# Kernel optimization log

Measured on AMD Instinct MI355X. Metric: run time of the kernel, lower is better.

## Reference

```python
import jax, jax.numpy as jnp
import numpy as np

NUM_HEADS = 8


def setup_inputs() -> dict:
    key = jax.random.key(0)
    k0, k1, k2 = jax.random.split(key, 3)
    B, C, D, H, W = 2, 256, 16, 16, 8
    x = jax.random.normal(k0, (B, C, D, H, W), dtype=jnp.float32)
    # 1x1x1 Conv3d weights are pointwise linear maps over channels
    w_qkv = jax.random.normal(k1, (3 * C, C), dtype=jnp.float32) * 0.02
    b_qkv = jnp.zeros((3 * C,), dtype=jnp.float32)
    w_out = jax.random.normal(k2, (C, C), dtype=jnp.float32) * 0.02
    b_out = jnp.zeros((C,), dtype=jnp.float32)
    return {"x": x, "w_qkv": w_qkv, "b_qkv": b_qkv, "w_out": w_out, "b_out": b_out}


def reference(x, w_qkv, b_qkv, w_out, b_out):
    b, c, d, h, w = x.shape
    nh = NUM_HEADS
    hd = c // nh
    scale = hd ** (-0.5)
    n = d * h * w
    xf = x.reshape(b, c, n)  # flatten spatial volume to N tokens
    # to_qkv: pointwise conv == channel-mixing matmul
    qkv = jnp.einsum('oc,bcn->bon', w_qkv, xf) + b_qkv[None, :, None]
    # torch: view(b, H, 3*hd, N) then chunk(3, dim=2) -> per-head channel grouping
    qkv = qkv.reshape(b, nh, 3 * hd, n)
    q, k, v = jnp.split(qkv, 3, axis=2)  # each (b, nh, hd, n)
    sim = jnp.einsum('bhcn,bhcm->bhnm', q, k) * scale  # (b, nh, N, N)
    attn = jax.nn.softmax(sim, axis=-1)
    out = jnp.einsum('bhnm,bhcm->bhcn', attn, v)  # (b, nh, hd, N)
    out = out.reshape(b, c, n)
    out = jnp.einsum('oc,bcn->bon', w_out, out) + b_out[None, :, None]
    return x + out.reshape(b, c, d, h, w)
```

## Files before the change

kernel.cpp:

```cpp
#include <hip/hip_runtime.h>
#include <hip/hip_bf16.h>
#include <math.h>

#define BB 2
#define CC 256
#define NH 8
#define HD 32
#define NN 2048
#define KSPAN 1024
#define QBLK 64
#define KTILE 64
#define NITER (KSPAN / KTILE)
#define QK_SCALE 0.25500917f

typedef __attribute__((ext_vector_type(8))) short short8;
typedef __attribute__((ext_vector_type(8))) unsigned short ushort8;
typedef __attribute__((ext_vector_type(4))) float f32x4;

__device__ inline unsigned short f2bf(float f) {
    __hip_bfloat16 h = __float2bfloat16(f);
    return __builtin_bit_cast(unsigned short, h);
}
__device__ inline int kperm(int k) {
    return 32 * (k >> 5) + 16 * ((k >> 2) & 1) + 4 * ((k >> 3) & 3) + (k & 3);
}
__device__ inline int xcd_chunk(int orig, int nwg) {
    int q = nwg >> 3, r = nwg & 7, x = orig & 7, s = orig >> 3;
    return (x < r ? x * (q + 1) : r * (q + 1) + (x - r) * q) + s;
}

__global__ __launch_bounds__(256) void qkv_mfma(const float* __restrict__ x,
                                                const float* __restrict__ wq,
                                                const float* __restrict__ bias,
                                                unsigned short* __restrict__ qt,
                                                unsigned short* __restrict__ ktt,
                                                unsigned short* __restrict__ vt) {
    const int l = xcd_chunk(blockIdx.x, 768);
    const int m0 = (l % 12) * 64;
    const int xtile = l / 12;
    const int n0 = (xtile & 31) * 64;
    const int b = xtile >> 5;
    const int t = threadIdx.x, lane = t & 63, wid = t >> 6;
    const int g = lane >> 4, ln = lane & 15;
    __shared__ __align__(16) unsigned short Aw[4][64][36];
    __shared__ __align__(16) unsigned short Bx[4][64][36];
    f32x4 acc[4] = {};

    const int sm = t & 63, sch = t >> 6;
    const int pc = t >> 4, pn = t & 15;
    const int c0 = pc * 8, nl = pn * 4;
    const float* xb = x + (size_t)b * CC * NN + n0;

    for (int kh = 0; kh < 2; ++kh) {
        __syncthreads();
        {
            const float* wsrc = wq + (size_t)(m0 + sm) * CC + kh * 128 + sch * 32;
            float wv[32];
#pragma unroll
            for (int j = 0; j < 8; ++j) *(float4*)&wv[j * 4] = *(const float4*)&wsrc[j * 4];
#pragma unroll
            for (int j2 = 0; j2 < 4; ++j2) {
                ushort8 p;
#pragma unroll
                for (int e = 0; e < 8; ++e) p[e] = f2bf(wv[j2 * 8 + e]);
                *(ushort8*)&Aw[sch][sm][j2 * 8] = p;
            }
        }
        {
            const float* xsrc = xb + (size_t)(kh * 128 + c0) * NN + nl;
            float xv[8][4];
#pragma unroll
            for (int i = 0; i < 8; ++i) *(float4*)&xv[i][0] = *(const float4*)&xsrc[(size_t)i * NN];
#pragma unroll
            for (int i2 = 0; i2 < 4; ++i2) {
                ushort8 p;
#pragma unroll
                for (int e = 0; e < 8; ++e) p[e] = f2bf(xv[e][i2]);
                *(ushort8*)&Bx[pc >> 2][nl + i2][(pc & 3) * 8] = p;
            }
        }
        __syncthreads();
#pragma unroll
        for (int ks = 0; ks < 4; ++ks) {
            short8 aW = *(const short8*)&Aw[ks][wid * 16 + ln][g * 8];
#pragma unroll
            for (int nt = 0; nt < 4; ++nt) {
                short8 bX = *(const short8*)&Bx[ks][nt * 16 + ln][g * 8];
                acc[nt] = __builtin_amdgcn_mfma_f32_16x16x32_bf16(aW, bX, acc[nt], 0, 0, 0);
            }
        }
    }
    __syncthreads();
    unsigned short (*Tqk)[64][40] = (unsigned short (*)[64][40])&Aw[0][0][0];
    unsigned short (*Tv)[32][72]  = (unsigned short (*)[32][72])&Bx[0][0][0];
    {
        const int grp = wid >> 1;
        const int cl0 = (wid & 1) * 16 + 4 * g;
        const int gm0 = m0 + grp * 32;
        const int gtype = (gm0 % 96) >> 5;
        const float sc = (gtype == 0) ? QK_SCALE : 1.0f;
        float bv[4];
#pragma unroll
        for (int r = 0; r < 4; ++r) bv[r] = bias[gm0 + cl0 + r];
        if (gtype == 2) {
#pragma unroll
            for (int nt = 0; nt < 4; ++nt)
#pragma unroll
                for (int r = 0; r < 4; ++r)
                    Tv[grp][cl0 + r][nt * 16 + ln] = f2bf(acc[nt][r] + bv[r]);
        } else {
#pragma unroll
            for (int nt = 0; nt < 4; ++nt)
#pragma unroll
                for (int r = 0; r < 4; ++r)
                    Tqk[grp][nt * 16 + ln][cl0 + r] = f2bf((acc[nt][r] + bv[r]) * sc);
        }
    }
    __syncthreads();
#pragma unroll
    for (int grp2 = 0; grp2 < 2; ++grp2) {
        const int gm = m0 + grp2 * 32;
        const int gtype = (gm % 96) >> 5;
        const int head = gm / 96;
        if (gtype == 2) {
            const int cl = t >> 3, n8 = (t & 7) * 8;
            ushort8 v = *(const ushort8*)&Tv[grp2][cl][n8];
            *(ushort8*)&vt[((size_t)(b * NH + head) * HD + cl) * NN + n0 + n8] = v;
        } else {
            unsigned short* dst = (gtype == 0) ? qt : ktt;
            const int nr = t >> 2, c8 = (t & 3) * 8;
            ushort8 v = *(const ushort8*)&Tqk[grp2][nr][c8];
            *(ushort8*)&dst[((size_t)(b * NH + head) * NN + n0 + nr) * HD + c8] = v;
        }
    }
}

__global__ __launch_bounds__(512) void attn_mfma(const unsigned short* __restrict__ Qt,
                                                 const unsigned short* __restrict__ Kt,
                                                 const unsigned short* __restrict__ Vt,
                                                 unsigned short* __restrict__ aout_t) {
    const int l = xcd_chunk(blockIdx.x, 512);
    const int n0 = (l & 31) * QBLK;
    const int bh = l >> 5;
    const int h = bh & 7, b = bh >> 3;
    const int t = threadIdx.x;
    const int lane = t & 63, wid = t >> 6;
    const int g = lane >> 4, ln = lane & 15;
    const int qg = wid & 3, whalf = wid >> 2;

    __shared__ __align__(16) unsigned short Qs[QBLK][40];
    __shared__ __align__(16) unsigned short Ks[2][2][KTILE][40];
    __shared__ __align__(16) unsigned short Vs[2][2][HD][72];

    const unsigned short* qb = Qt + ((size_t)(b * NH + h) * NN + n0) * HD;
    const unsigned short* kb = Kt + (size_t)(b * NH + h) * NN * HD;
    const unsigned short* vb = Vt + (size_t)(b * NH + h) * HD * NN;

    if (t < 256) {
        int q = t >> 2, ch = (t & 3) * 8;
        *(ushort8*)&Qs[q][ch] = *(const ushort8*)&qb[(size_t)q * HD + ch];
    }
    __syncthreads();
    const short8 bQ = *(const short8*)&Qs[qg * 16 + ln][g * 8];

    const int th = t & 255, sthalf = t >> 8;
    const int sk = th >> 2, sch = (th & 3) * 8;
    const int rowK = kperm(sk);
    const int vcc = th >> 3, vn = (th & 7) * 8;
    const size_t hbase = (size_t)sthalf * KSPAN;

    ushort8 kpreA = *(const ushort8*)&kb[(hbase + 0 * KTILE + sk) * HD + sch];
    ushort8 vpreA = *(const ushort8*)&vb[(size_t)vcc * NN + hbase + 0 * KTILE + vn];
    ushort8 kpreB = *(const ushort8*)&kb[(hbase + 1 * KTILE + sk) * HD + sch];
    ushort8 vpreB = *(const ushort8*)&vb[(size_t)vcc * NN + hbase + 1 * KTILE + vn];

    float l_run = 0.f;
    f32x4 oacc[2];
    const f32x4 zero4 = {0.f, 0.f, 0.f, 0.f};
    oacc[0] = zero4; oacc[1] = zero4;

    auto compute_tile = [&](int buf) {
        f32x4 sacc[4];
        __builtin_amdgcn_s_setprio(1);
#pragma unroll
        for (int t8 = 0; t8 < 4; ++t8) {
            short8 aK = *(const short8*)&Ks[whalf][buf][t8 * 16 + ln][g * 8];
            sacc[t8] = __builtin_amdgcn_mfma_f32_16x16x32_bf16(aK, bQ, zero4, 0, 0, 0);
        }
        __builtin_amdgcn_s_setprio(0);

#pragma unroll
        for (int t8 = 0; t8 < 4; ++t8) {
            sacc[t8][0] = exp2f(sacc[t8][0]);
            sacc[t8][1] = exp2f(sacc[t8][1]);
            sacc[t8][2] = exp2f(sacc[t8][2]);
            sacc[t8][3] = exp2f(sacc[t8][3]);
        }
        float ps[4];
#pragma unroll
        for (int t8 = 0; t8 < 4; ++t8)
            ps[t8] = (sacc[t8][0] + sacc[t8][1]) + (sacc[t8][2] + sacc[t8][3]);
        l_run += (ps[0] + ps[1]) + (ps[2] + ps[3]);

        short8 aP[2];
#pragma unroll
        for (int kc = 0; kc < 2; ++kc)
#pragma unroll
            for (int u = 0; u < 2; ++u)
#pragma unroll
                for (int r = 0; r < 4; ++r)
                    aP[kc][u * 4 + r] = (short)f2bf(sacc[2 * kc + u][r]);

        __builtin_amdgcn_s_setprio(1);
#pragma unroll
        for (int kc = 0; kc < 2; ++kc) {
            short8 bV0 = *(const short8*)&Vs[whalf][buf][ln][kc * 32 + g * 8];
            short8 bV1 = *(const short8*)&Vs[whalf][buf][16 + ln][kc * 32 + g * 8];
            oacc[0] = __builtin_amdgcn_mfma_f32_16x16x32_bf16(aP[kc], bV0, oacc[0], 0, 0, 0);
            oacc[1] = __builtin_amdgcn_mfma_f32_16x16x32_bf16(aP[kc], bV1, oacc[1], 0, 0, 0);
        }
        __builtin_amdgcn_s_setprio(0);
    };

    for (int it = 0; it < NITER; it += 2) {
        *(ushort8*)&Ks[sthalf][0][rowK][sch] = kpreA;
        *(ushort8*)&Vs[sthalf][0][vcc][vn]   = vpreA;
        if (it + 2 < NITER) {
            size_t kt = hbase + (size_t)(it + 2) * KTILE;
            kpreA = *(const ushort8*)&kb[(kt + sk) * HD + sch];
            vpreA = *(const ushort8*)&vb[(size_t)vcc * NN + kt + vn];
        }
        __syncthreads();
        compute_tile(0);
        *(ushort8*)&Ks[sthalf][1][rowK][sch] = kpreB;
        *(ushort8*)&Vs[sthalf][1][vcc][vn]   = vpreB;
        if (it + 3 < NITER) {
            size_t kt = hbase + (size_t)(it + 3) * KTILE;
            kpreB = *(const ushort8*)&kb[(kt + sk) * HD + sch];
            vpreB = *(const ushort8*)&vb[(size_t)vcc * NN + kt + vn];
        }
        __syncthreads();
        compute_tile(1);
    }

    l_run += __shfl_xor(l_run, 16);
    l_run += __shfl_xor(l_run, 32);

    __syncthreads();
    float* Of  = (float*)&Ks[0][0][0][0];
    float* Ls  = (float*)&Vs[0][0][0][0];
#pragma unroll
    for (int ct = 0; ct < 2; ++ct)
#pragma unroll
        for (int r = 0; r < 4; ++r)
            Of[((whalf * 64) + qg * 16 + 4 * g + r) * 40 + ct * 16 + ln] = oacc[ct][r];
    if (g == 0) Ls[whalf * 64 + qg * 16 + ln] = l_run;
    __syncthreads();
    {
        const int q = t >> 3, c0 = (t & 7) * 4;
        f32x4 o0 = *(const f32x4*)&Of[(size_t)q * 40 + c0];
        f32x4 o1 = *(const f32x4*)&Of[(size_t)(64 + q) * 40 + c0];
        float dinv = 1.0f / (Ls[q] + Ls[64 + q]);
        ushort4 r4;
        r4.x = f2bf((o0[0] + o1[0]) * dinv);
        r4.y = f2bf((o0[1] + o1[1]) * dinv);
        r4.z = f2bf((o0[2] + o1[2]) * dinv);
        r4.w = f2bf((o0[3] + o1[3]) * dinv);
        *(ushort4*)&aout_t[((size_t)b * NN + n0 + q) * CC + h * HD + c0] = r4;
    }
}

__global__ __launch_bounds__(256) void proj_mfma(const unsigned short* __restrict__ aout_t,
                                                 const float* __restrict__ wo,
                                                 const float* __restrict__ bias,
                                                 const float* __restrict__ x,
                                                 float* __restrict__ out) {
    const int l = xcd_chunk(blockIdx.x, 512);
    const int n0 = (l & 63) * 32;
    const int bm = l >> 6;
    const int m0 = (bm & 3) * 64, b = bm >> 2;
    const int t = threadIdx.x, lane = t & 63, wid = t >> 6;
    const int g = lane >> 4, ln = lane & 15;
    __shared__ __align__(16) unsigned short Aw[4][64][36];
    __shared__ __align__(16) unsigned short Bx[4][32][36];
    f32x4 acc[2] = {};
    const unsigned short* ab = aout_t + ((size_t)b * NN + n0) * CC;

    const int sm = t & 63, sch = t >> 6;
    const int bn = t & 31, bch = t >> 5;
    for (int kh = 0; kh < 2; ++kh) {
        __syncthreads();
        {
            const float* wsrc = wo + (size_t)(m0 + sm) * CC + kh * 128 + sch * 32;
            float wv[32];
#pragma unroll
            for (int j = 0; j < 8; ++j) *(float4*)&wv[j * 4] = *(const float4*)&wsrc[j * 4];
#pragma unroll
            for (int j2 = 0; j2 < 4; ++j2) {
                ushort8 p;
#pragma unroll
                for (int e = 0; e < 8; ++e) p[e] = f2bf(wv[j2 * 8 + e]);
                *(ushort8*)&Aw[sch][sm][j2 * 8] = p;
            }
        }
        {
            int ks = bch >> 1, off = (bch & 1) * 16;
            const unsigned short* src = &ab[(size_t)bn * CC + kh * 128 + ks * 32 + off];
            *(ushort8*)&Bx[ks][bn][off]     = *(const ushort8*)&src[0];
            *(ushort8*)&Bx[ks][bn][off + 8] = *(const ushort8*)&src[8];
        }
        __syncthreads();
#pragma unroll
        for (int ks = 0; ks < 4; ++ks) {
            short8 aW = *(const short8*)&Aw[ks][wid * 16 + ln][g * 8];
#pragma unroll
            for (int nt = 0; nt < 2; ++nt) {
                short8 bX = *(const short8*)&Bx[ks][nt * 16 + ln][g * 8];
                acc[nt] = __builtin_amdgcn_mfma_f32_16x16x32_bf16(aW, bX, acc[nt], 0, 0, 0);
            }
        }
    }
    const int mbase = m0 + wid * 16 + 4 * g;
    float bv[4];
#pragma unroll
    for (int r = 0; r < 4; ++r) bv[r] = bias[mbase + r];
#pragma unroll
    for (int nt = 0; nt < 2; ++nt) {
        int n = n0 + nt * 16 + ln;
#pragma unroll
        for (int r = 0; r < 4; ++r) {
            size_t off = ((size_t)b * CC + mbase + r) * NN + n;
            out[off] = acc[nt][r] + bv[r] + x[off];
        }
    }
}

extern "C" void kernel_launch(void* const* d_in, const int* in_sizes, int n_in,
                              void* d_out, int out_size, void* d_ws, size_t ws_size,
                              hipStream_t stream) {
    const float* x     = (const float*)d_in[0];
    const float* w_qkv = (const float*)d_in[1];
    const float* b_qkv = (const float*)d_in[2];
    const float* w_out = (const float*)d_in[3];
    const float* b_out = (const float*)d_in[4];
    float* out = (float*)d_out;

    unsigned short* qt     = (unsigned short*)d_ws;
    unsigned short* ktt    = qt  + (size_t)BB * NH * NN * HD;
    unsigned short* vt     = ktt + (size_t)BB * NH * NN * HD;
    unsigned short* aout_t = vt  + (size_t)BB * NH * NN * HD;

    qkv_mfma<<<dim3(768), 256, 0, stream>>>(x, w_qkv, b_qkv, qt, ktt, vt);
    attn_mfma<<<dim3(512), 512, 0, stream>>>(qt, ktt, vt, aout_t);
    proj_mfma<<<dim3(512), 256, 0, stream>>>(aout_t, w_out, b_out, x, out);
}
```

Baseline: 47.44 us.

## Split attention keys across all eight waves with direct register loads and LDS reduction

The attention kernel now gives each of the 8 waves a disjoint 256-key slice covering all 64 queries. K and V fragments are read straight from global memory into registers, replacing the double-buffered LDS staging and its per-tile barriers. Partial outputs and row sums are then combined across waves through shared memory in two channel halves. This removes the shared-memory round trips and synchronisation in the main loop. In exchange it uses more accumulator registers, issues uncoalesced fragment-shaped global loads, and adds an 8-way LDS reduction at the end.

```diff
diff --git a/kernel.cpp b/kernel.cpp
--- a/kernel.cpp
+++ b/kernel.cpp
@@ -7,10 +7,7 @@
 #define NH 8
 #define HD 32
 #define NN 2048
-#define KSPAN 1024
 #define QBLK 64
-#define KTILE 64
-#define NITER (KSPAN / KTILE)
 #define QK_SCALE 0.25500917f
 
 typedef __attribute__((ext_vector_type(8))) short short8;
@@ -20,9 +17,6 @@
 __device__ inline unsigned short f2bf(float f) {
     __hip_bfloat16 h = __float2bfloat16(f);
     return __builtin_bit_cast(unsigned short, h);
-}
-__device__ inline int kperm(int k) {
-    return 32 * (k >> 5) + 16 * ((k >> 2) & 1) + 4 * ((k >> 3) & 3) + (k & 3);
 }
 __device__ inline int xcd_chunk(int orig, int nwg) {
     int q = nwg >> 3, r = nwg & 7, x = orig & 7, s = orig >> 3;
@@ -135,138 +129,122 @@
     }
 }
 
-__global__ __launch_bounds__(512) void attn_mfma(const unsigned short* __restrict__ Qt,
-                                                 const unsigned short* __restrict__ Kt,
-                                                 const unsigned short* __restrict__ Vt,
-                                                 unsigned short* __restrict__ aout_t) {
+__global__ __launch_bounds__(512, 4) void attn_mfma(const unsigned short* __restrict__ Qt,
+                                                    const unsigned short* __restrict__ Kt,
+                                                    const unsigned short* __restrict__ Vt,
+                                                    unsigned short* __restrict__ aout_t) {
     const int l = xcd_chunk(blockIdx.x, 512);
     const int n0 = (l & 31) * QBLK;
     const int bh = l >> 5;
     const int h = bh & 7, b = bh >> 3;
     const int t = threadIdx.x;
-    const int lane = t & 63, wid = t >> 6;
+    const int lane = t & 63, w = t >> 6;
     const int g = lane >> 4, ln = lane & 15;
-    const int qg = wid & 3, whalf = wid >> 2;
-
-    __shared__ __align__(16) unsigned short Qs[QBLK][40];
-    __shared__ __align__(16) unsigned short Ks[2][2][KTILE][40];
-    __shared__ __align__(16) unsigned short Vs[2][2][HD][72];
+
+    __shared__ float Of[8][64][18];
+    __shared__ float Ls[8][64];
 
     const unsigned short* qb = Qt + ((size_t)(b * NH + h) * NN + n0) * HD;
     const unsigned short* kb = Kt + (size_t)(b * NH + h) * NN * HD;
     const unsigned short* vb = Vt + (size_t)(b * NH + h) * HD * NN;
 
-    if (t < 256) {
-        int q = t >> 2, ch = (t & 3) * 8;
-        *(ushort8*)&Qs[q][ch] = *(const ushort8*)&qb[(size_t)q * HD + ch];
-    }
-    __syncthreads();
-    const short8 bQ = *(const short8*)&Qs[qg * 16 + ln][g * 8];
-
-    const int th = t & 255, sthalf = t >> 8;
-    const int sk = th >> 2, sch = (th & 3) * 8;
-    const int rowK = kperm(sk);
-    const int vcc = th >> 3, vn = (th & 7) * 8;
-    const size_t hbase = (size_t)sthalf * KSPAN;
-
-    ushort8 kpreA = *(const ushort8*)&kb[(hbase + 0 * KTILE + sk) * HD + sch];
-    ushort8 vpreA = *(const ushort8*)&vb[(size_t)vcc * NN + hbase + 0 * KTILE + vn];
-    ushort8 kpreB = *(const ushort8*)&kb[(hbase + 1 * KTILE + sk) * HD + sch];
-    ushort8 vpreB = *(const ushort8*)&vb[(size_t)vcc * NN + hbase + 1 * KTILE + vn];
-
-    float l_run = 0.f;
-    f32x4 oacc[2];
+    short8 bQ[4];
+#pragma unroll
+    for (int qt = 0; qt < 4; ++qt)
+        bQ[qt] = *(const short8*)&qb[(size_t)(qt * 16 + ln) * HD + g * 8];
+
+    const int krow = 8 * (ln >> 2) + (ln & 3);
+    const int wkey0 = w * 256;
+
+    f32x4 oacc[4][2];
     const f32x4 zero4 = {0.f, 0.f, 0.f, 0.f};
-    oacc[0] = zero4; oacc[1] = zero4;
-
-    auto compute_tile = [&](int buf) {
-        f32x4 sacc[4];
+#pragma unroll
+    for (int qt = 0; qt < 4; ++qt) { oacc[qt][0] = zero4; oacc[qt][1] = zero4; }
+    float l_run[4] = {0.f, 0.f, 0.f, 0.f};
+
+    short8 kA0 = *(const short8*)&kb[(size_t)(wkey0 + krow + 0) * HD + g * 8];
+    short8 kA1 = *(const short8*)&kb[(size_t)(wkey0 + krow + 4) * HD + g * 8];
+
+    for (int it = 0; it < 8; ++it) {
+        const int kt0 = wkey0 + it * 32;
+        short8 bV0 = *(const short8*)&vb[(size_t)ln * NN + kt0 + g * 8];
+        short8 bV1 = *(const short8*)&vb[(size_t)(16 + ln) * NN + kt0 + g * 8];
+
+        f32x4 sacc[2][4];
         __builtin_amdgcn_s_setprio(1);
 #pragma unroll
-        for (int t8 = 0; t8 < 4; ++t8) {
-            short8 aK = *(const short8*)&Ks[whalf][buf][t8 * 16 + ln][g * 8];
-            sacc[t8] = __builtin_amdgcn_mfma_f32_16x16x32_bf16(aK, bQ, zero4, 0, 0, 0);
+        for (int qt = 0; qt < 4; ++qt) {
+            sacc[0][qt] = __builtin_amdgcn_mfma_f32_16x16x32_bf16(kA0, bQ[qt], zero4, 0, 0, 0);
+            sacc[1][qt] = __builtin_amdgcn_mfma_f32_16x16x32_bf16(kA1, bQ[qt], zero4, 0, 0, 0);
         }
         __builtin_amdgcn_s_setprio(0);
 
-#pragma unroll
-        for (int t8 = 0; t8 < 4; ++t8) {
-            sacc[t8][0] = exp2f(sacc[t8][0]);
-            sacc[t8][1] = exp2f(sacc[t8][1]);
-            sacc[t8][2] = exp2f(sacc[t8][2]);
-            sacc[t8][3] = exp2f(sacc[t8][3]);
-        }
-        float ps[4];
-#pragma unroll
-        for (int t8 = 0; t8 < 4; ++t8)
-            ps[t8] = (sacc[t8][0] + sacc[t8][1]) + (sacc[t8][2] + sacc[t8][3]);
-        l_run += (ps[0] + ps[1]) + (ps[2] + ps[3]);
-
-        short8 aP[2];
-#pragma unroll
-        for (int kc = 0; kc < 2; ++kc)
-#pragma unroll
-            for (int u = 0; u < 2; ++u)
-#pragma unroll
-                for (int r = 0; r < 4; ++r)
-                    aP[kc][u * 4 + r] = (short)f2bf(sacc[2 * kc + u][r]);
+        if (it + 1 < 8) {
+            kA0 = *(const short8*)&kb[(size_t)(kt0 + 32 + krow + 0) * HD + g * 8];
+            kA1 = *(const short8*)&kb[(size_t)(kt0 + 32 + krow + 4) * HD + g * 8];
+        }
+
+        short8 aP[4];
+#pragma unroll
+        for (int qt = 0; qt < 4; ++qt) {
+#pragma unroll
+            for (int u = 0; u < 2; ++u) {
+#pragma unroll
+                for (int r = 0; r < 4; ++r) {
+                    float p = exp2f(sacc[u][qt][r]);
+                    sacc[u][qt][r] = p;
+                    aP[qt][u * 4 + r] = (short)f2bf(p);
+                }
+            }
+            l_run[qt] += ((sacc[0][qt][0] + sacc[0][qt][1]) + (sacc[0][qt][2] + sacc[0][qt][3]))
+                       + ((sacc[1][qt][0] + sacc[1][qt][1]) + (sacc[1][qt][2] + sacc[1][qt][3]));
+        }
 
         __builtin_amdgcn_s_setprio(1);
 #pragma unroll
-        for (int kc = 0; kc < 2; ++kc) {
-            short8 bV0 = *(const short8*)&Vs[whalf][buf][ln][kc * 32 + g * 8];
-            short8 bV1 = *(const short8*)&Vs[whalf][buf][16 + ln][kc * 32 + g * 8];
-            oacc[0] = __builtin_amdgcn_mfma_f32_16x16x32_bf16(aP[kc], bV0, oacc[0], 0, 0, 0);
-            oacc[1] = __builtin_amdgcn_mfma_f32_16x16x32_bf16(aP[kc], bV1, oacc[1], 0, 0, 0);
+        for (int qt = 0; qt < 4; ++qt) {
+            oacc[qt][0] = __builtin_amdgcn_mfma_f32_16x16x32_bf16(aP[qt], bV0, oacc[qt][0], 0, 0, 0);
+            oacc[qt][1] = __builtin_amdgcn_mfma_f32_16x16x32_bf16(aP[qt], bV1, oacc[qt][1], 0, 0, 0);
         }
         __builtin_amdgcn_s_setprio(0);
-    };
-
-    for (int it = 0; it < NITER; it += 2) {
-        *(ushort8*)&Ks[sthalf][0][rowK][sch] = kpreA;
-        *(ushort8*)&Vs[sthalf][0][vcc][vn]   = vpreA;
-        if (it + 2 < NITER) {
-            size_t kt = hbase + (size_t)(it + 2) * KTILE;
-            kpreA = *(const ushort8*)&kb[(kt + sk) * HD + sch];
-            vpreA = *(const ushort8*)&vb[(size_t)vcc * NN + kt + vn];
-        }
-        __syncthreads();
-        compute_tile(0);
-        *(ushort8*)&Ks[sthalf][1][rowK][sch] = kpreB;
-        *(ushort8*)&Vs[sthalf][1][vcc][vn]   = vpreB;
-        if (it + 3 < NITER) {
-            size_t kt = hbase + (size_t)(it + 3) * KTILE;
-            kpreB = *(const ushort8*)&kb[(kt + sk) * HD + sch];
-            vpreB = *(const ushort8*)&vb[(size_t)vcc * NN + kt + vn];
-        }
-        __syncthreads();
-        compute_tile(1);
-    }
-
-    l_run += __shfl_xor(l_run, 16);
-    l_run += __shfl_xor(l_run, 32);
-
-    __syncthreads();
-    float* Of  = (float*)&Ks[0][0][0][0];
-    float* Ls  = (float*)&Vs[0][0][0][0];
-#pragma unroll
-    for (int ct = 0; ct < 2; ++ct)
-#pragma unroll
-        for (int r = 0; r < 4; ++r)
-            Of[((whalf * 64) + qg * 16 + 4 * g + r) * 40 + ct * 16 + ln] = oacc[ct][r];
-    if (g == 0) Ls[whalf * 64 + qg * 16 + ln] = l_run;
-    __syncthreads();
-    {
-        const int q = t >> 3, c0 = (t & 7) * 4;
-        f32x4 o0 = *(const f32x4*)&Of[(size_t)q * 40 + c0];
-        f32x4 o1 = *(const f32x4*)&Of[(size_t)(64 + q) * 40 + c0];
-        float dinv = 1.0f / (Ls[q] + Ls[64 + q]);
-        ushort4 r4;
-        r4.x = f2bf((o0[0] + o1[0]) * dinv);
-        r4.y = f2bf((o0[1] + o1[1]) * dinv);
-        r4.z = f2bf((o0[2] + o1[2]) * dinv);
-        r4.w = f2bf((o0[3] + o1[3]) * dinv);
-        *(ushort4*)&aout_t[((size_t)b * NN + n0 + q) * CC + h * HD + c0] = r4;
+    }
+
+#pragma unroll
+    for (int qt = 0; qt < 4; ++qt) {
+        l_run[qt] += __shfl_xor(l_run[qt], 16);
+        l_run[qt] += __shfl_xor(l_run[qt], 32);
+    }
+
+    const int rq = t >> 3, c2 = (t & 7) * 2;
+    float linv = 0.f;
+#pragma unroll
+    for (int ch = 0; ch < 2; ++ch) {
+        if (ch) __syncthreads();
+#pragma unroll
+        for (int qt = 0; qt < 4; ++qt)
+#pragma unroll
+            for (int r = 0; r < 4; ++r)
+                Of[w][qt * 16 + 4 * g + r][ln] = oacc[qt][ch][r];
+        if (ch == 0 && g == 0)
+#pragma unroll
+            for (int qt = 0; qt < 4; ++qt) Ls[w][qt * 16 + ln] = l_run[qt];
+        __syncthreads();
+        float s0 = 0.f, s1 = 0.f;
+#pragma unroll
+        for (int ww = 0; ww < 8; ++ww) {
+            s0 += Of[ww][rq][c2];
+            s1 += Of[ww][rq][c2 + 1];
+        }
+        if (ch == 0) {
+            float lsum = 0.f;
+#pragma unroll
+            for (int ww = 0; ww < 8; ++ww) lsum += Ls[ww][rq];
+            linv = 1.0f / lsum;
+        }
+        ushort2 r2;
+        r2.x = f2bf(s0 * linv);
+        r2.y = f2bf(s1 * linv);
+        *(ushort2*)&aout_t[((size_t)b * NN + n0 + rq) * CC + h * HD + ch * 16 + c2] = r2;
     }
 }
 
```

Measured after the change: 46.49 us. 2.0% less time.
